# Optimization experiments

Measured on AMD Instinct MI355X. Metric: run time of the kernel, lower is better.

## Reference

```python
import jax, jax.numpy as jnp
import numpy as np

N_NODES = 100000
N_EDGES = 1600000
IN_DIM = 128
HEADS = 8
NEG_SLOPE = 0.2  # PyG GATConv default


def _glorot(key, shape):
    fan_in, fan_out = shape[0], shape[-1]
    lim = jnp.sqrt(6.0 / (fan_in + fan_out))
    return jax.random.uniform(key, shape, jnp.float32, -lim, lim)


def setup_inputs() -> dict:
    key = jax.random.key(0)
    ks = jax.random.split(key, 20)
    x = jax.random.normal(ks[0], (N_NODES, IN_DIM), jnp.float32)
    edge_index = jax.random.randint(ks[1], (2, N_EDGES), 0, N_NODES, jnp.int32)
    # layer 1: 128 -> 8 heads x 16
    W1 = _glorot(ks[2], (128, 128)); a_src1 = _glorot(ks[3], (8, 16)); a_dst1 = _glorot(ks[4], (8, 16)); b1 = jnp.zeros((128,), jnp.float32)
    # layer 2: 128 -> 8 heads x 16
    W2 = _glorot(ks[5], (128, 128)); a_src2 = _glorot(ks[6], (8, 16)); a_dst2 = _glorot(ks[7], (8, 16)); b2 = jnp.zeros((128,), jnp.float32)
    # layer 3: 128 -> 1 head x 64, concat=False (mean)
    W3 = _glorot(ks[8], (128, 64)); a_src3 = _glorot(ks[9], (1, 64)); a_dst3 = _glorot(ks[10], (1, 64)); b3 = jnp.zeros((64,), jnp.float32)
    Wout = _glorot(ks[11], (64, 2)); bout = jnp.zeros((2,), jnp.float32)
    return {"x": x, "edge_index": edge_index,
            "W1": W1, "a_src1": a_src1, "a_dst1": a_dst1, "b1": b1,
            "W2": W2, "a_src2": a_src2, "a_dst2": a_dst2, "b2": b2,
            "W3": W3, "a_src3": a_src3, "a_dst3": a_dst3, "b3": b3,
            "Wout": Wout, "bout": bout}


def gat_conv(x, src, dst, W, a_src, a_dst, bias, concat):
    """PyG-style GATConv (eval mode, self-loops already appended to src/dst)."""
    n = x.shape[0]
    H, C = a_src.shape
    h = (x @ W).reshape(n, H, C)                        # [N,H,C]
    alpha_src = jnp.einsum('nhc,hc->nh', h, a_src)       # [N,H]
    alpha_dst = jnp.einsum('nhc,hc->nh', h, a_dst)       # [N,H]
    e = jax.nn.leaky_relu(alpha_src[src] + alpha_dst[dst], NEG_SLOPE)  # [E,H]
    # segment softmax over incoming edges of each destination node
    m = jax.ops.segment_max(e, dst, num_segments=n)      # [N,H]
    ex = jnp.exp(e - m[dst])
    denom = jax.ops.segment_sum(ex, dst, num_segments=n)  # [N,H]
    alpha = ex / (denom[dst] + 1e-16)                    # [E,H]
    # weighted gather-scatter aggregation
    msg = alpha[:, :, None] * h[src]                     # [E,H,C]
    out = jax.ops.segment_sum(msg, dst, num_segments=n)  # [N,H,C]
    out = out.reshape(n, H * C) if concat else out.mean(axis=1)
    return out + bias


def reference(x, edge_index, W1, a_src1, a_dst1, b1, W2, a_src2, a_dst2, b2,
              W3, a_src3, a_dst3, b3, Wout, bout):
    n = x.shape[0]
    loops = jnp.arange(n, dtype=edge_index.dtype)
    src = jnp.concatenate([edge_index[0], loops])
    dst = jnp.concatenate([edge_index[1], loops])
    h = jax.nn.elu(gat_conv(x, src, dst, W1, a_src1, a_dst1, b1, concat=True))
    h = jax.nn.elu(gat_conv(h, src, dst, W2, a_src2, a_dst2, b2, concat=True))
    h = jax.nn.elu(gat_conv(h, src, dst, W3, a_src3, a_dst3, b3, concat=False))
    return h @ Wout + bout
```

## Files before the change

kernel.cpp:

```cpp
#include <hip/hip_runtime.h>
#include <math.h>

#define NN 100000
#define NE 1600000
#define ET (NE + NN)
#define SCAN_BLK 4096

typedef __attribute__((ext_vector_type(8))) short bf16x8;
typedef __attribute__((ext_vector_type(4))) float f32x4;

__device__ inline unsigned short f2bf(float f) {
  union { float f; unsigned u; } v; v.f = f;
  unsigned r = v.u + 0x7fffu + ((v.u >> 16) & 1u);
  return (unsigned short)(r >> 16);
}
__device__ inline float bflo(unsigned u) { union { unsigned u; float f; } v; v.u = u << 16; return v.f; }
__device__ inline float bfhi(unsigned u) { union { unsigned u; float f; } v; v.u = u & 0xffff0000u; return v.f; }
__device__ inline float bfs(unsigned short u) { union { unsigned u; float f; } v; v.u = ((unsigned)u) << 16; return v.f; }

__global__ __launch_bounds__(256) void k_hist(const int* __restrict__ dst, int* __restrict__ counts,
                                              int* __restrict__ slots) {
  int base = blockIdx.x * 2048 + threadIdx.x;
#pragma unroll
  for (int j = 0; j < 8; ++j) {
    int i = base + j * 256;
    if (i < ET) {
      int d = (i < NE) ? dst[i] : (i - NE);
      slots[i] = atomicAdd(&counts[d], 1);
    }
  }
}

__global__ __launch_bounds__(256) void k_scan1(const int* __restrict__ counts, int* __restrict__ partial,
                                               int* __restrict__ blksum) {
  __shared__ int lds[256];
  int b = blockIdx.x, t = threadIdx.x;
  int base = b * SCAN_BLK + t * 16;
  int v[16];
  int s = 0;
#pragma unroll
  for (int j = 0; j < 16; j++) {
    int x = (base + j < NN) ? counts[base + j] : 0;
    s += x; v[j] = s;
  }
  lds[t] = s; __syncthreads();
  int tot = s;
  for (int off = 1; off < 256; off <<= 1) {
    int u = 0; if (t >= off) u = lds[t - off];
    __syncthreads(); lds[t] += u; __syncthreads();
  }
  int pre = lds[t] - tot;
#pragma unroll
  for (int j = 0; j < 16; j++) if (base + j < NN) partial[base + j] = pre + v[j];
  if (t == 255) blksum[b] = lds[255];
}

__global__ __launch_bounds__(256) void k_scan2(int* __restrict__ blksum, int nb) {
  __shared__ int lds[256];
  int t = threadIdx.x;
  int v = (t < nb) ? blksum[t] : 0;
  lds[t] = v; __syncthreads();
  for (int off = 1; off < 256; off <<= 1) {
    int u = 0; if (t >= off) u = lds[t - off];
    __syncthreads(); lds[t] += u; __syncthreads();
  }
  if (t < nb) blksum[t] = lds[t] - v;
}

__global__ __launch_bounds__(256) void k_scan3(const int* __restrict__ partial, const int* __restrict__ blksum,
                                               int* __restrict__ rowptr) {
  int i = blockIdx.x * 256 + threadIdx.x;
  if (i >= NN) return;
  rowptr[i + 1] = partial[i] + blksum[i / SCAN_BLK];
  if (i == 0) rowptr[0] = 0;
}

__global__ __launch_bounds__(256) void k_scatter(const int* __restrict__ src, const int* __restrict__ dst,
                                                 const int* __restrict__ rowptr, const int* __restrict__ slots,
                                                 int* __restrict__ esrc) {
  int base = blockIdx.x * 2048 + threadIdx.x;
#pragma unroll
  for (int j = 0; j < 8; ++j) {
    int i = base + j * 256;
    if (i < ET) {
      int d, s;
      if (i < NE) { d = dst[i]; s = src[i]; } else { d = i - NE; s = d; }
      esrc[rowptr[d] + slots[i]] = s;
    }
  }
}

template<int M, bool XBF>
__global__ __launch_bounds__(256) void k_gemm(const float* __restrict__ Xf, const unsigned short* __restrict__ Xb,
                                              const float* __restrict__ W,
                                              const float* __restrict__ a_src, const float* __restrict__ a_dst,
                                              unsigned short* __restrict__ Hf, float* __restrict__ as_, float* __restrict__ ad_) {
  constexpr int NCBW = M / 64;
  __shared__ __attribute__((aligned(16))) unsigned short xs[64 * 136];
  __shared__ __attribute__((aligned(16))) unsigned short wt[M * 136];
  __shared__ float asl[M], adl[M];
  const int t = threadIdx.x;
  const int wave = t >> 6, l = t & 63;
  const int lr = l & 15, kg = l >> 4;
  const int wc0 = wave * (M / 4);
  const int row0 = blockIdx.x * 64;

  if constexpr (XBF) {
#pragma unroll
    for (int p = 0; p < 4; ++p) {
      int f = p * 256 + t;
      int row = f >> 4, ch = f & 15;
      uint4 v = make_uint4(0, 0, 0, 0);
      if (row0 + row < NN) v = *(const uint4*)(Xb + (size_t)(row0 + row) * 128 + ch * 8);
      *(uint4*)(xs + row * 136 + ch * 8) = v;
    }
  } else {
#pragma unroll
    for (int p = 0; p < 8; ++p) {
      int f = p * 256 + t;
      int row = f >> 5, ch = f & 31;
      float4 v = make_float4(0.f, 0.f, 0.f, 0.f);
      if (row0 + row < NN) v = *(const float4*)(Xf + (size_t)(row0 + row) * 128 + ch * 4);
      uint2 pk;
      pk.x = (unsigned)f2bf(v.x) | ((unsigned)f2bf(v.y) << 16);
      pk.y = (unsigned)f2bf(v.z) | ((unsigned)f2bf(v.w) << 16);
      *(uint2*)(xs + row * 136 + ch * 4) = pk;
    }
  }
#pragma unroll
  for (int p = 0; p < M / 8; ++p) {
    int f = p * 256 + t;
    int k = f & 127, cg = f >> 7;
    float4 v = *(const float4*)(W + (size_t)k * M + cg * 4);
    wt[(cg * 4 + 0) * 136 + k] = f2bf(v.x);
    wt[(cg * 4 + 1) * 136 + k] = f2bf(v.y);
    wt[(cg * 4 + 2) * 136 + k] = f2bf(v.z);
    wt[(cg * 4 + 3) * 136 + k] = f2bf(v.w);
  }
  if (t < M) { asl[t] = a_src[t]; adl[t] = a_dst[t]; }
  __syncthreads();

  f32x4 acc[4][NCBW];
#pragma unroll
  for (int rb = 0; rb < 4; ++rb)
#pragma unroll
    for (int cb = 0; cb < NCBW; ++cb) acc[rb][cb] = (f32x4){0.f, 0.f, 0.f, 0.f};
#pragma unroll
  for (int kb = 0; kb < 4; ++kb) {
    bf16x8 af[4], bfr[NCBW];
#pragma unroll
    for (int rb = 0; rb < 4; ++rb)
      af[rb] = *(const bf16x8*)(xs + (rb * 16 + lr) * 136 + kb * 32 + kg * 8);
#pragma unroll
    for (int cb = 0; cb < NCBW; ++cb)
      bfr[cb] = *(const bf16x8*)(wt + (size_t)(wc0 + cb * 16 + lr) * 136 + kb * 32 + kg * 8);
#pragma unroll
    for (int rb = 0; rb < 4; ++rb)
#pragma unroll
      for (int cb = 0; cb < NCBW; ++cb)
        acc[rb][cb] = __builtin_amdgcn_mfma_f32_16x16x32_bf16(af[rb], bfr[cb], acc[rb][cb], 0, 0, 0);
  }

  __syncthreads();
#pragma unroll
  for (int rb = 0; rb < 4; ++rb)
#pragma unroll
    for (int cb = 0; cb < NCBW; ++cb)
#pragma unroll
      for (int r = 0; r < 4; ++r) {
        int row = rb * 16 + kg * 4 + r;
        int col = wc0 + cb * 16 + lr;
        xs[row * 136 + col] = f2bf(acc[rb][cb][r]);
      }
  __syncthreads();

  if constexpr (M == 128) {
    int row = t >> 2, cg = t & 3;
    int gr = row0 + row;
    if (gr < NN) {
#pragma unroll
      for (int j = 0; j < 4; ++j)
        *(uint4*)(Hf + (size_t)gr * 128 + cg * 32 + j * 8) = *(const uint4*)(xs + row * 136 + cg * 32 + j * 8);
#pragma unroll
      for (int hi = 0; hi < 2; ++hi) {
        int hh = cg * 2 + hi;
        uint4 u0 = *(const uint4*)(xs + row * 136 + hh * 16);
        uint4 u1 = *(const uint4*)(xs + row * 136 + hh * 16 + 8);
        float hv[16] = {bflo(u0.x), bfhi(u0.x), bflo(u0.y), bfhi(u0.y),
                        bflo(u0.z), bfhi(u0.z), bflo(u0.w), bfhi(u0.w),
                        bflo(u1.x), bfhi(u1.x), bflo(u1.y), bfhi(u1.y),
                        bflo(u1.z), bfhi(u1.z), bflo(u1.w), bfhi(u1.w)};
        float s1 = 0.f, s2 = 0.f;
#pragma unroll
        for (int j = 0; j < 16; ++j) { s1 += hv[j] * asl[hh * 16 + j]; s2 += hv[j] * adl[hh * 16 + j]; }
        as_[(size_t)gr * 8 + hh] = s1;
        ad_[(size_t)gr * 8 + hh] = s2;
      }
    }
  } else {
    int row = t >> 2, q = t & 3;
    int gr = row0 + row;
    uint4 u0 = *(const uint4*)(xs + row * 136 + q * 16);
    uint4 u1 = *(const uint4*)(xs + row * 136 + q * 16 + 8);
    float hv[16] = {bflo(u0.x), bfhi(u0.x), bflo(u0.y), bfhi(u0.y),
                    bflo(u0.z), bfhi(u0.z), bflo(u0.w), bfhi(u0.w),
                    bflo(u1.x), bfhi(u1.x), bflo(u1.y), bfhi(u1.y),
                    bflo(u1.z), bfhi(u1.z), bflo(u1.w), bfhi(u1.w)};
    float s1 = 0.f, s2 = 0.f;
#pragma unroll
    for (int j = 0; j < 16; ++j) { s1 += hv[j] * asl[q * 16 + j]; s2 += hv[j] * adl[q * 16 + j]; }
    s1 += __shfl_xor(s1, 1); s1 += __shfl_xor(s1, 2);
    s2 += __shfl_xor(s2, 1); s2 += __shfl_xor(s2, 2);
    if (gr < NN) {
      *(uint4*)(Hf + (size_t)gr * 64 + q * 16)     = u0;
      *(uint4*)(Hf + (size_t)gr * 64 + q * 16 + 8) = u1;
      if (q == 0) { as_[gr] = s1; ad_[gr] = s2; }
    }
  }
}

template<int HH, int C, bool FINAL>
__global__ __launch_bounds__(256) void k_aggregate(const unsigned short* __restrict__ Hf,
                                                   const float* __restrict__ as_, const float* __restrict__ ad_,
                                                   const int* __restrict__ rowptr, const int* __restrict__ esrc,
                                                   const float* __restrict__ bias,
                                                   const float* __restrict__ Wout, const float* __restrict__ bout,
                                                   unsigned short* __restrict__ outb, float* __restrict__ outf) {
  constexpr int CT = HH * C;
  constexpr int Q = CT / 8;
  int g = blockIdx.x * 256 + threadIdx.x;
  if (g >= NN * Q) return;
  int node = g / Q;
  int q = g - node * Q;
  int c = q * 8;
  int hh = c / C;
  int i0 = rowptr[node], i1 = rowptr[node + 1];
  float ad = ad_[node * HH + hh];
  float d[4] = {0.f, 0.f, 0.f, 0.f};
  float a[4][8] = {};
  int i = i0;
  for (; i + 3 < i1; i += 4) {
    int sx[4]; float ex[4]; uint4 hx[4];
#pragma unroll
    for (int c4 = 0; c4 < 4; ++c4) sx[c4] = esrc[i + c4];
#pragma unroll
    for (int c4 = 0; c4 < 4; ++c4) ex[c4] = as_[sx[c4] * HH + hh] + ad;
#pragma unroll
    for (int c4 = 0; c4 < 4; ++c4) hx[c4] = *(const uint4*)(Hf + (size_t)sx[c4] * CT + c);
#pragma unroll
    for (int c4 = 0; c4 < 4; ++c4) {
      float e = fmaxf(ex[c4], 0.2f * ex[c4]);
      float pp = __expf(e);
      d[c4] += pp;
      a[c4][0] = fmaf(pp, bflo(hx[c4].x), a[c4][0]);
      a[c4][1] = fmaf(pp, bfhi(hx[c4].x), a[c4][1]);
      a[c4][2] = fmaf(pp, bflo(hx[c4].y), a[c4][2]);
      a[c4][3] = fmaf(pp, bfhi(hx[c4].y), a[c4][3]);
      a[c4][4] = fmaf(pp, bflo(hx[c4].z), a[c4][4]);
      a[c4][5] = fmaf(pp, bfhi(hx[c4].z), a[c4][5]);
      a[c4][6] = fmaf(pp, bflo(hx[c4].w), a[c4][6]);
      a[c4][7] = fmaf(pp, bfhi(hx[c4].w), a[c4][7]);
    }
  }
  for (; i < i1; ++i) {
    int s = esrc[i];
    float e = as_[s * HH + hh] + ad;
    uint4 h0 = *(const uint4*)(Hf + (size_t)s * CT + c);
    e = fmaxf(e, 0.2f * e);
    float pp = __expf(e);
    d[0] += pp;
    a[0][0] = fmaf(pp, bflo(h0.x), a[0][0]);
    a[0][1] = fmaf(pp, bfhi(h0.x), a[0][1]);
    a[0][2] = fmaf(pp, bflo(h0.y), a[0][2]);
    a[0][3] = fmaf(pp, bfhi(h0.y), a[0][3]);
    a[0][4] = fmaf(pp, bflo(h0.z), a[0][4]);
    a[0][5] = fmaf(pp, bfhi(h0.z), a[0][5]);
    a[0][6] = fmaf(pp, bflo(h0.w), a[0][6]);
    a[0][7] = fmaf(pp, bfhi(h0.w), a[0][7]);
  }
  float inv = 1.f / (d[0] + d[1] + d[2] + d[3]);
  float o[8];
#pragma unroll
  for (int j = 0; j < 8; ++j) {
    float v = (a[0][j] + a[1][j] + a[2][j] + a[3][j]) * inv + bias[c + j];
    o[j] = v > 0.f ? v : __expf(v) - 1.f;
  }
  if constexpr (!FINAL) {
    uint4 pk;
    pk.x = (unsigned)f2bf(o[0]) | ((unsigned)f2bf(o[1]) << 16);
    pk.y = (unsigned)f2bf(o[2]) | ((unsigned)f2bf(o[3]) << 16);
    pk.z = (unsigned)f2bf(o[4]) | ((unsigned)f2bf(o[5]) << 16);
    pk.w = (unsigned)f2bf(o[6]) | ((unsigned)f2bf(o[7]) << 16);
    *(uint4*)(outb + (size_t)node * CT + c) = pk;
  } else {
    float p0 = 0.f, p1 = 0.f;
#pragma unroll
    for (int j = 0; j < 8; ++j) { p0 += o[j] * Wout[(c + j) * 2 + 0]; p1 += o[j] * Wout[(c + j) * 2 + 1]; }
#pragma unroll
    for (int off = 1; off < 8; off <<= 1) { p0 += __shfl_xor(p0, off); p1 += __shfl_xor(p1, off); }
    if (q == 0) { outf[node * 2 + 0] = p0 + bout[0]; outf[node * 2 + 1] = p1 + bout[1]; }
  }
}

extern "C" void kernel_launch(void* const* d_in, const int* in_sizes, int n_in,
                              void* d_out, int out_size, void* d_ws, size_t ws_size,
                              hipStream_t stream) {
  const float* x    = (const float*)d_in[0];
  const int*   ei   = (const int*)d_in[1];
  const float* W1   = (const float*)d_in[2];
  const float* as1  = (const float*)d_in[3];
  const float* ad1  = (const float*)d_in[4];
  const float* b1   = (const float*)d_in[5];
  const float* W2   = (const float*)d_in[6];
  const float* as2  = (const float*)d_in[7];
  const float* ad2  = (const float*)d_in[8];
  const float* b2   = (const float*)d_in[9];
  const float* W3   = (const float*)d_in[10];
  const float* as3  = (const float*)d_in[11];
  const float* ad3  = (const float*)d_in[12];
  const float* b3   = (const float*)d_in[13];
  const float* Wout = (const float*)d_in[14];
  const float* bout = (const float*)d_in[15];
  const int* srcp = ei;
  const int* dstp = ei + NE;

  char* p = (char*)d_ws;
  auto alloc = [&](size_t bytes) { char* r = p; p += (bytes + 255) & ~size_t(255); return r; };
  int*            rowptr  = (int*)alloc((size_t)(NN + 1) * 4);
  int*            counts  = (int*)alloc((size_t)NN * 4);
  int*            partial = (int*)alloc((size_t)NN * 4);
  int*            blksum  = (int*)alloc(256 * 4);
  int*            esrc    = (int*)alloc((size_t)ET * 4);
  int*            slots   = (int*)alloc((size_t)ET * 4);
  float*          asb     = (float*)alloc((size_t)NN * 8 * 4);
  float*          adb     = (float*)alloc((size_t)NN * 8 * 4);
  unsigned short* hfb     = (unsigned short*)alloc((size_t)NN * 128 * 2);
  unsigned short* actb    = (unsigned short*)alloc((size_t)NN * 128 * 2);

  hipMemsetAsync(counts, 0, (size_t)NN * 4, stream);
  int gE8 = (ET + 2047) / 2048;
  int nb = (NN + SCAN_BLK - 1) / SCAN_BLK;
  k_hist<<<gE8, 256, 0, stream>>>(dstp, counts, slots);
  k_scan1<<<nb, 256, 0, stream>>>(counts, partial, blksum);
  k_scan2<<<1, 256, 0, stream>>>(blksum, nb);
  k_scan3<<<(NN + 255) / 256, 256, 0, stream>>>(partial, blksum, rowptr);
  k_scatter<<<gE8, 256, 0, stream>>>(srcp, dstp, rowptr, slots, esrc);

  int gGemm = (NN + 63) / 64;
  k_gemm<128, false><<<gGemm, 256, 0, stream>>>(x, nullptr, W1, as1, ad1, hfb, asb, adb);
  k_aggregate<8, 16, false><<<(NN * 16 + 255) / 256, 256, 0, stream>>>(hfb, asb, adb, rowptr, esrc, b1, nullptr, nullptr, actb, nullptr);
  k_gemm<128, true><<<gGemm, 256, 0, stream>>>(nullptr, actb, W2, as2, ad2, hfb, asb, adb);
  k_aggregate<8, 16, false><<<(NN * 16 + 255) / 256, 256, 0, stream>>>(hfb, asb, adb, rowptr, esrc, b2, nullptr, nullptr, actb, nullptr);
  k_gemm<64, true><<<gGemm, 256, 0, stream>>>(nullptr, actb, W3, as3, ad3, hfb, asb, adb);
  k_aggregate<1, 64, true><<<(NN * 8 + 255) / 256, 256, 0, stream>>>(hfb, asb, adb, rowptr, esrc, b3, Wout, bout, nullptr, (float*)d_out);
}
```

Before: 388.9 us.

## Fuse layer aggregation with next layer's GEMM into one kernel

Adds a k_aggemm kernel that aggregates 64 destination nodes into shared memory as bf16 and then multiplies that tile by the next layer's weight with MFMA, also computing the attention logits. It replaces two aggregate-plus-GEMM kernel pairs, removing the round trip of the intermediate activation through global memory and two launches, with ping-pong buffers for the inputs and outputs. The aggregation inner loop is cut from 4-way to 2-way unrolling, and hist/scatter blocks now process 16 elements per thread instead of 8. The risks are lower occupancy from larger shared memory use, fewer blocks doing the gather, and the weight tile being reloaded from global memory in two K halves.

```diff
diff --git a/kernel.cpp b/kernel.cpp
--- a/kernel.cpp
+++ b/kernel.cpp
@@ -16,13 +16,12 @@
 }
 __device__ inline float bflo(unsigned u) { union { unsigned u; float f; } v; v.u = u << 16; return v.f; }
 __device__ inline float bfhi(unsigned u) { union { unsigned u; float f; } v; v.u = u & 0xffff0000u; return v.f; }
-__device__ inline float bfs(unsigned short u) { union { unsigned u; float f; } v; v.u = ((unsigned)u) << 16; return v.f; }
 
 __global__ __launch_bounds__(256) void k_hist(const int* __restrict__ dst, int* __restrict__ counts,
                                               int* __restrict__ slots) {
-  int base = blockIdx.x * 2048 + threadIdx.x;
-#pragma unroll
-  for (int j = 0; j < 8; ++j) {
+  int base = blockIdx.x * 4096 + threadIdx.x;
+#pragma unroll
+  for (int j = 0; j < 16; ++j) {
     int i = base + j * 256;
     if (i < ET) {
       int d = (i < NE) ? dst[i] : (i - NE);
@@ -78,9 +77,9 @@
 __global__ __launch_bounds__(256) void k_scatter(const int* __restrict__ src, const int* __restrict__ dst,
                                                  const int* __restrict__ rowptr, const int* __restrict__ slots,
                                                  int* __restrict__ esrc) {
-  int base = blockIdx.x * 2048 + threadIdx.x;
-#pragma unroll
-  for (int j = 0; j < 8; ++j) {
+  int base = blockIdx.x * 4096 + threadIdx.x;
+#pragma unroll
+  for (int j = 0; j < 16; ++j) {
     int i = base + j * 256;
     if (i < ET) {
       int d, s;
@@ -215,6 +214,213 @@
       *(uint4*)(Hf + (size_t)gr * 64 + q * 16)     = u0;
       *(uint4*)(Hf + (size_t)gr * 64 + q * 16 + 8) = u1;
       if (q == 0) { as_[gr] = s1; ad_[gr] = s2; }
+    }
+  }
+}
+
+template<int M>
+__global__ __launch_bounds__(256) void k_aggemm(
+    const unsigned short* __restrict__ HfIn, const float* __restrict__ asIn, const float* __restrict__ adIn,
+    const int* __restrict__ rowptr, const int* __restrict__ esrc, const float* __restrict__ bias,
+    const float* __restrict__ W, const float* __restrict__ a_src, const float* __restrict__ a_dst,
+    unsigned short* __restrict__ HfOut, float* __restrict__ asOut, float* __restrict__ adOut) {
+  constexpr int NCBW = M / 64;
+  __shared__ __attribute__((aligned(16))) unsigned short xs[64 * 136];
+  __shared__ __attribute__((aligned(16))) unsigned short wt[M * 72];
+  __shared__ float asl[M], adl[M];
+  const int t = threadIdx.x;
+  const int wave = t >> 6, l = t & 63;
+  const int lr = l & 15, kg = l >> 4;
+  const int wc0 = wave * (M / 4);
+  const int row0 = blockIdx.x * 64;
+
+  {
+    constexpr int PT = (M * 64 / 4) / 256;
+#pragma unroll
+    for (int p = 0; p < PT; ++p) {
+      int f = p * 256 + t;
+      int k = f / (M / 4), cg = f % (M / 4);
+      float4 v = *(const float4*)(W + (size_t)k * M + cg * 4);
+      wt[(cg * 4 + 0) * 72 + k] = f2bf(v.x);
+      wt[(cg * 4 + 1) * 72 + k] = f2bf(v.y);
+      wt[(cg * 4 + 2) * 72 + k] = f2bf(v.z);
+      wt[(cg * 4 + 3) * 72 + k] = f2bf(v.w);
+    }
+  }
+  if (t < M) { asl[t] = a_src[t]; adl[t] = a_dst[t]; }
+
+#pragma unroll
+  for (int jj = 0; jj < 4; ++jj) {
+    int j = jj * 256 + t;
+    int nl = j >> 4, q = j & 15;
+    int node = row0 + nl;
+    int c = q * 8, hh = q >> 1;
+    float o[8];
+    if (node < NN) {
+      int i0 = rowptr[node], i1 = rowptr[node + 1];
+      float ad = adIn[node * 8 + hh];
+      float d0 = 0.f, d1 = 0.f;
+      float a0[8] = {}, a1[8] = {};
+      int i = i0;
+      for (; i + 1 < i1; i += 2) {
+        int sA = esrc[i], sB = esrc[i + 1];
+        float eA = asIn[sA * 8 + hh] + ad;
+        float eB = asIn[sB * 8 + hh] + ad;
+        uint4 hA = *(const uint4*)(HfIn + (size_t)sA * 128 + c);
+        uint4 hB = *(const uint4*)(HfIn + (size_t)sB * 128 + c);
+        eA = fmaxf(eA, 0.2f * eA);
+        eB = fmaxf(eB, 0.2f * eB);
+        float pA = __expf(eA), pB = __expf(eB);
+        d0 += pA;                             d1 += pB;
+        a0[0] = fmaf(pA, bflo(hA.x), a0[0]);  a1[0] = fmaf(pB, bflo(hB.x), a1[0]);
+        a0[1] = fmaf(pA, bfhi(hA.x), a0[1]);  a1[1] = fmaf(pB, bfhi(hB.x), a1[1]);
+        a0[2] = fmaf(pA, bflo(hA.y), a0[2]);  a1[2] = fmaf(pB, bflo(hB.y), a1[2]);
+        a0[3] = fmaf(pA, bfhi(hA.y), a0[3]);  a1[3] = fmaf(pB, bfhi(hB.y), a1[3]);
+        a0[4] = fmaf(pA, bflo(hA.z), a0[4]);  a1[4] = fmaf(pB, bflo(hB.z), a1[4]);
+        a0[5] = fmaf(pA, bfhi(hA.z), a0[5]);  a1[5] = fmaf(pB, bfhi(hB.z), a1[5]);
+        a0[6] = fmaf(pA, bflo(hA.w), a0[6]);  a1[6] = fmaf(pB, bflo(hB.w), a1[6]);
+        a0[7] = fmaf(pA, bfhi(hA.w), a0[7]);  a1[7] = fmaf(pB, bfhi(hB.w), a1[7]);
+      }
+      if (i < i1) {
+        int sA = esrc[i];
+        float eA = asIn[sA * 8 + hh] + ad;
+        uint4 hA = *(const uint4*)(HfIn + (size_t)sA * 128 + c);
+        eA = fmaxf(eA, 0.2f * eA);
+        float pA = __expf(eA);
+        d0 += pA;
+        a0[0] = fmaf(pA, bflo(hA.x), a0[0]);
+        a0[1] = fmaf(pA, bfhi(hA.x), a0[1]);
+        a0[2] = fmaf(pA, bflo(hA.y), a0[2]);
+        a0[3] = fmaf(pA, bfhi(hA.y), a0[3]);
+        a0[4] = fmaf(pA, bflo(hA.z), a0[4]);
+        a0[5] = fmaf(pA, bfhi(hA.z), a0[5]);
+        a0[6] = fmaf(pA, bflo(hA.w), a0[6]);
+        a0[7] = fmaf(pA, bfhi(hA.w), a0[7]);
+      }
+      float inv = 1.f / (d0 + d1);
+#pragma unroll
+      for (int jx = 0; jx < 8; ++jx) {
+        float v = (a0[jx] + a1[jx]) * inv + bias[c + jx];
+        o[jx] = v > 0.f ? v : __expf(v) - 1.f;
+      }
+    } else {
+#pragma unroll
+      for (int jx = 0; jx < 8; ++jx) o[jx] = 0.f;
+    }
+    uint4 pk;
+    pk.x = (unsigned)f2bf(o[0]) | ((unsigned)f2bf(o[1]) << 16);
+    pk.y = (unsigned)f2bf(o[2]) | ((unsigned)f2bf(o[3]) << 16);
+    pk.z = (unsigned)f2bf(o[4]) | ((unsigned)f2bf(o[5]) << 16);
+    pk.w = (unsigned)f2bf(o[6]) | ((unsigned)f2bf(o[7]) << 16);
+    *(uint4*)(xs + nl * 136 + c) = pk;
+  }
+  __syncthreads();
+
+  f32x4 acc[4][NCBW];
+#pragma unroll
+  for (int rb = 0; rb < 4; ++rb)
+#pragma unroll
+    for (int cb = 0; cb < NCBW; ++cb) acc[rb][cb] = (f32x4){0.f, 0.f, 0.f, 0.f};
+#pragma unroll
+  for (int kb = 0; kb < 2; ++kb) {
+    bf16x8 af[4], bfr[NCBW];
+#pragma unroll
+    for (int rb = 0; rb < 4; ++rb)
+      af[rb] = *(const bf16x8*)(xs + (rb * 16 + lr) * 136 + kb * 32 + kg * 8);
+#pragma unroll
+    for (int cb = 0; cb < NCBW; ++cb)
+      bfr[cb] = *(const bf16x8*)(wt + (size_t)(wc0 + cb * 16 + lr) * 72 + kb * 32 + kg * 8);
+#pragma unroll
+    for (int rb = 0; rb < 4; ++rb)
+#pragma unroll
+      for (int cb = 0; cb < NCBW; ++cb)
+        acc[rb][cb] = __builtin_amdgcn_mfma_f32_16x16x32_bf16(af[rb], bfr[cb], acc[rb][cb], 0, 0, 0);
+  }
+  __syncthreads();
+  {
+    constexpr int PT = (M * 64 / 4) / 256;
+#pragma unroll
+    for (int p = 0; p < PT; ++p) {
+      int f = p * 256 + t;
+      int k = f / (M / 4), cg = f % (M / 4);
+      float4 v = *(const float4*)(W + (size_t)(k + 64) * M + cg * 4);
+      wt[(cg * 4 + 0) * 72 + k] = f2bf(v.x);
+      wt[(cg * 4 + 1) * 72 + k] = f2bf(v.y);
+      wt[(cg * 4 + 2) * 72 + k] = f2bf(v.z);
+      wt[(cg * 4 + 3) * 72 + k] = f2bf(v.w);
+    }
+  }
+  __syncthreads();
+#pragma unroll
+  for (int kb = 0; kb < 2; ++kb) {
+    bf16x8 af[4], bfr[NCBW];
+#pragma unroll
+    for (int rb = 0; rb < 4; ++rb)
+      af[rb] = *(const bf16x8*)(xs + (rb * 16 + lr) * 136 + (kb + 2) * 32 + kg * 8);
+#pragma unroll
+    for (int cb = 0; cb < NCBW; ++cb)
+      bfr[cb] = *(const bf16x8*)(wt + (size_t)(wc0 + cb * 16 + lr) * 72 + kb * 32 + kg * 8);
+#pragma unroll
+    for (int rb = 0; rb < 4; ++rb)
+#pragma unroll
+      for (int cb = 0; cb < NCBW; ++cb)
+        acc[rb][cb] = __builtin_amdgcn_mfma_f32_16x16x32_bf16(af[rb], bfr[cb], acc[rb][cb], 0, 0, 0);
+  }
+  __syncthreads();
+
+#pragma unroll
+  for (int rb = 0; rb < 4; ++rb)
+#pragma unroll
+    for (int cb = 0; cb < NCBW; ++cb)
+#pragma unroll
+      for (int r = 0; r < 4; ++r) {
+        int row = rb * 16 + kg * 4 + r;
+        int col = wc0 + cb * 16 + lr;
+        xs[row * 136 + col] = f2bf(acc[rb][cb][r]);
+      }
+  __syncthreads();
+
+  if constexpr (M == 128) {
+    int row = t >> 2, cg = t & 3;
+    int gr = row0 + row;
+    if (gr < NN) {
+#pragma unroll
+      for (int j = 0; j < 4; ++j)
+        *(uint4*)(HfOut + (size_t)gr * 128 + cg * 32 + j * 8) = *(const uint4*)(xs + row * 136 + cg * 32 + j * 8);
+#pragma unroll
+      for (int hi = 0; hi < 2; ++hi) {
+        int hh = cg * 2 + hi;
+        uint4 u0 = *(const uint4*)(xs + row * 136 + hh * 16);
+        uint4 u1 = *(const uint4*)(xs + row * 136 + hh * 16 + 8);
+        float hv[16] = {bflo(u0.x), bfhi(u0.x), bflo(u0.y), bfhi(u0.y),
+                        bflo(u0.z), bfhi(u0.z), bflo(u0.w), bfhi(u0.w),
+                        bflo(u1.x), bfhi(u1.x), bflo(u1.y), bfhi(u1.y),
+                        bflo(u1.z), bfhi(u1.z), bflo(u1.w), bfhi(u1.w)};
+        float s1 = 0.f, s2 = 0.f;
+#pragma unroll
+        for (int j = 0; j < 16; ++j) { s1 += hv[j] * asl[hh * 16 + j]; s2 += hv[j] * adl[hh * 16 + j]; }
+        asOut[(size_t)gr * 8 + hh] = s1;
+        adOut[(size_t)gr * 8 + hh] = s2;
+      }
+    }
+  } else {
+    int row = t >> 2, q = t & 3;
+    int gr = row0 + row;
+    uint4 u0 = *(const uint4*)(xs + row * 136 + q * 16);
+    uint4 u1 = *(const uint4*)(xs + row * 136 + q * 16 + 8);
+    float hv[16] = {bflo(u0.x), bfhi(u0.x), bflo(u0.y), bfhi(u0.y),
+                    bflo(u0.z), bfhi(u0.z), bflo(u0.w), bfhi(u0.w),
+                    bflo(u1.x), bfhi(u1.x), bflo(u1.y), bfhi(u1.y),
+                    bflo(u1.z), bfhi(u1.z), bflo(u1.w), bfhi(u1.w)};
+    float s1 = 0.f, s2 = 0.f;
+#pragma unroll
+    for (int j = 0; j < 16; ++j) { s1 += hv[j] * asl[q * 16 + j]; s2 += hv[j] * adl[q * 16 + j]; }
+    s1 += __shfl_xor(s1, 1); s1 += __shfl_xor(s1, 2);
+    s2 += __shfl_xor(s2, 1); s2 += __shfl_xor(s2, 2);
+    if (gr < NN) {
+      *(uint4*)(HfOut + (size_t)gr * 64 + q * 16)     = u0;
+      *(uint4*)(HfOut + (size_t)gr * 64 + q * 16 + 8) = u1;
+      if (q == 0) { asOut[gr] = s1; adOut[gr] = s2; }
     }
   }
 }
@@ -236,53 +442,49 @@
   int hh = c / C;
   int i0 = rowptr[node], i1 = rowptr[node + 1];
   float ad = ad_[node * HH + hh];
-  float d[4] = {0.f, 0.f, 0.f, 0.f};
-  float a[4][8] = {};
+  float d0 = 0.f, d1 = 0.f;
+  float a0[8] = {}, a1[8] = {};
   int i = i0;
-  for (; i + 3 < i1; i += 4) {
-    int sx[4]; float ex[4]; uint4 hx[4];
-#pragma unroll
-    for (int c4 = 0; c4 < 4; ++c4) sx[c4] = esrc[i + c4];
-#pragma unroll
-    for (int c4 = 0; c4 < 4; ++c4) ex[c4] = as_[sx[c4] * HH + hh] + ad;
-#pragma unroll
-    for (int c4 = 0; c4 < 4; ++c4) hx[c4] = *(const uint4*)(Hf + (size_t)sx[c4] * CT + c);
-#pragma unroll
-    for (int c4 = 0; c4 < 4; ++c4) {
-      float e = fmaxf(ex[c4], 0.2f * ex[c4]);
-      float pp = __expf(e);
-      d[c4] += pp;
-      a[c4][0] = fmaf(pp, bflo(hx[c4].x), a[c4][0]);
-      a[c4][1] = fmaf(pp, bfhi(hx[c4].x), a[c4][1]);
-      a[c4][2] = fmaf(pp, bflo(hx[c4].y), a[c4][2]);
-      a[c4][3] = fmaf(pp, bfhi(hx[c4].y), a[c4][3]);
-      a[c4][4] = fmaf(pp, bflo(hx[c4].z), a[c4][4]);
-      a[c4][5] = fmaf(pp, bfhi(hx[c4].z), a[c4][5]);
-      a[c4][6] = fmaf(pp, bflo(hx[c4].w), a[c4][6]);
-      a[c4][7] = fmaf(pp, bfhi(hx[c4].w), a[c4][7]);
-    }
-  }
-  for (; i < i1; ++i) {
-    int s = esrc[i];
-    float e = as_[s * HH + hh] + ad;
-    uint4 h0 = *(const uint4*)(Hf + (size_t)s * CT + c);
-    e = fmaxf(e, 0.2f * e);
-    float pp = __expf(e);
-    d[0] += pp;
-    a[0][0] = fmaf(pp, bflo(h0.x), a[0][0]);
-    a[0][1] = fmaf(pp, bfhi(h0.x), a[0][1]);
-    a[0][2] = fmaf(pp, bflo(h0.y), a[0][2]);
-    a[0][3] = fmaf(pp, bfhi(h0.y), a[0][3]);
-    a[0][4] = fmaf(pp, bflo(h0.z), a[0][4]);
-    a[0][5] = fmaf(pp, bfhi(h0.z), a[0][5]);
-    a[0][6] = fmaf(pp, bflo(h0.w), a[0][6]);
-    a[0][7] = fmaf(pp, bfhi(h0.w), a[0][7]);
-  }
-  float inv = 1.f / (d[0] + d[1] + d[2] + d[3]);
+  for (; i + 1 < i1; i += 2) {
+    int sA = esrc[i], sB = esrc[i + 1];
+    float eA = as_[sA * HH + hh] + ad;
+    float eB = as_[sB * HH + hh] + ad;
+    uint4 hA = *(const uint4*)(Hf + (size_t)sA * CT + c);
+    uint4 hB = *(const uint4*)(Hf + (size_t)sB * CT + c);
+    eA = fmaxf(eA, 0.2f * eA);
+    eB = fmaxf(eB, 0.2f * eB);
+    float pA = __expf(eA), pB = __expf(eB);
+    d0 += pA;                             d1 += pB;
+    a0[0] = fmaf(pA, bflo(hA.x), a0[0]);  a1[0] = fmaf(pB, bflo(hB.x), a1[0]);
+    a0[1] = fmaf(pA, bfhi(hA.x), a0[1]);  a1[1] = fmaf(pB, bfhi(hB.x), a1[1]);
+    a0[2] = fmaf(pA, bflo(hA.y), a0[2]);  a1[2] = fmaf(pB, bflo(hB.y), a1[2]);
+    a0[3] = fmaf(pA, bfhi(hA.y), a0[3]);  a1[3] = fmaf(pB, bfhi(hB.y), a1[3]);
+    a0[4] = fmaf(pA, bflo(hA.z), a0[4]);  a1[4] = fmaf(pB, bflo(hB.z), a1[4]);
+    a0[5] = fmaf(pA, bfhi(hA.z), a0[5]);  a1[5] = fmaf(pB, bfhi(hB.z), a1[5]);
+    a0[6] = fmaf(pA, bflo(hA.w), a0[6]);  a1[6] = fmaf(pB, bflo(hB.w), a1[6]);
+    a0[7] = fmaf(pA, bfhi(hA.w), a0[7]);  a1[7] = fmaf(pB, bfhi(hB.w), a1[7]);
+  }
+  if (i < i1) {
+    int sA = esrc[i];
+    float eA = as_[sA * HH + hh] + ad;
+    uint4 hA = *(const uint4*)(Hf + (size_t)sA * CT + c);
+    eA = fmaxf(eA, 0.2f * eA);
+    float pA = __expf(eA);
+    d0 += pA;
+    a0[0] = fmaf(pA, bflo(hA.x), a0[0]);
+    a0[1] = fmaf(pA, bfhi(hA.x), a0[1]);
+    a0[2] = fmaf(pA, bflo(hA.y), a0[2]);
+    a0[3] = fmaf(pA, bfhi(hA.y), a0[3]);
+    a0[4] = fmaf(pA, bflo(hA.z), a0[4]);
+    a0[5] = fmaf(pA, bfhi(hA.z), a0[5]);
+    a0[6] = fmaf(pA, bflo(hA.w), a0[6]);
+    a0[7] = fmaf(pA, bfhi(hA.w), a0[7]);
+  }
+  float inv = 1.f / (d0 + d1);
   float o[8];
 #pragma unroll
   for (int j = 0; j < 8; ++j) {
-    float v = (a[0][j] + a[1][j] + a[2][j] + a[3][j]) * inv + bias[c + j];
+    float v = (a0[j] + a1[j]) * inv + bias[c + j];
     o[j] = v > 0.f ? v : __expf(v) - 1.f;
   }
   if constexpr (!FINAL) {
@@ -332,25 +534,25 @@
   int*            blksum  = (int*)alloc(256 * 4);
   int*            esrc    = (int*)alloc((size_t)ET * 4);
   int*            slots   = (int*)alloc((size_t)ET * 4);
-  float*          asb     = (float*)alloc((size_t)NN * 8 * 4);
-  float*          adb     = (float*)alloc((size_t)NN * 8 * 4);
-  unsigned short* hfb     = (unsigned short*)alloc((size_t)NN * 128 * 2);
-  unsigned short* actb    = (unsigned short*)alloc((size_t)NN * 128 * 2);
+  float*          asbA    = (float*)alloc((size_t)NN * 8 * 4);
+  float*          adbA    = (float*)alloc((size_t)NN * 8 * 4);
+  float*          asbB    = (float*)alloc((size_t)NN * 8 * 4);
+  float*          adbB    = (float*)alloc((size_t)NN * 8 * 4);
+  unsigned short* hfA     = (unsigned short*)alloc((size_t)NN * 128 * 2);
+  unsigned short* hfB     = (unsigned short*)alloc((size_t)NN * 128 * 2);
 
   hipMemsetAsync(counts, 0, (size_t)NN * 4, stream);
-  int gE8 = (ET + 2047) / 2048;
+  int gE16 = (ET + 4095) / 4096;
   int nb = (NN + SCAN_BLK - 1) / SCAN_BLK;
-  k_hist<<<gE8, 256, 0, stream>>>(dstp, counts, slots);
+  k_hist<<<gE16, 256, 0, stream>>>(dstp, counts, slots);
   k_scan1<<<nb, 256, 0, stream>>>(counts, partial, blksum);
   k_scan2<<<1, 256, 0, stream>>>(blksum, nb);
   k_scan3<<<(NN + 255) / 256, 256, 0, stream>>>(partial, blksum, rowptr);
-  k_scatter<<<gE8, 256, 0, stream>>>(srcp, dstp, rowptr, slots, esrc);
+  k_scatter<<<gE16, 256, 0, stream>>>(srcp, dstp, rowptr, slots, esrc);
 
   int gGemm = (NN + 63) / 64;
-  k_gemm<128, false><<<gGemm, 256, 0, stream>>>(x, nullptr, W1, as1, ad1, hfb, asb, adb);
-  k_aggregate<8, 16, false><<<(NN * 16 + 255) / 256, 256, 0, stream>>>(hfb, asb, adb, rowptr, esrc, b1, nullptr, nullptr, actb, nullptr);
-  k_gemm<128, true><<<gGemm, 256, 0, stream>>>(nullptr, actb, W2, as2, ad2, hfb, asb, adb);
-  k_aggregate<8, 16, false><<<(NN * 16 + 255) / 256, 256, 0, stream>>>(hfb, asb, adb, rowptr, esrc, b2, nullptr, nullptr, actb, nullptr);
-  k_gemm<64, true><<<gGemm, 256, 0, stream>>>(nullptr, actb, W3, as3, ad3, hfb, asb, adb);
-  k_aggregate<1, 64, true><<<(NN * 8 + 255) / 256, 256, 0, stream>>>(hfb, asb, adb, rowptr, esrc, b3, Wout, bout, nullptr, (float*)d_out);
-}
+  k_gemm<128, false><<<gGemm, 256, 0, stream>>>(x, nullptr, W1, as1, ad1, hfA, asbA, adbA);
+  k_aggemm<128><<<gGemm, 256, 0, stream>>>(hfA, asbA, adbA, rowptr, esrc, b1, W2, as2, ad2, hfB, asbB, adbB);
+  k_aggemm<64><<<gGemm, 256, 0, stream>>>(hfB, asbB, adbB, rowptr, esrc, b2, W3, as3, ad3, hfA, asbA, adbA);
+  k_aggregate<1, 64, true><<<(NN * 8 + 255) / 256, 256, 0, stream>>>(hfA, asbA, adbA, rowptr, esrc, b3, Wout, bout, nullptr, (float*)d_out);
+}
```

Measured after the change: 400.2 us. 1.03x slower.
